# Optimization experiments

Measured on AMD Instinct MI355X. Metric: run time of the kernel, lower is better.

Reference implementation:

```python
import jax, jax.numpy as jnp
import numpy as np

N_NODES = 50000
N_EDGES = 800000
IN_CH = 128
HID = 64
NUM_HEADS = 8
NUM_CLASSES = 2
NEG_SLOPE = 0.2   # PyG GATConv default LeakyReLU slope
BN_EPS = 1e-5
SOFTMAX_EPS = 1e-16  # PyG softmax denominator epsilon


def setup_inputs() -> dict:
    key = jax.random.key(0)
    ks = jax.random.split(key, 20)
    s = 0.1
    inp = {
        "x": jax.random.normal(ks[0], (N_NODES, IN_CH), dtype=jnp.float32),
        "edge_index": jax.random.randint(ks[1], (2, N_EDGES), 0, N_NODES, dtype=jnp.int64),
        # layer 0 params, stacked over the 8 independent heads
        "W0": jax.random.normal(ks[2], (NUM_HEADS, IN_CH, HID), dtype=jnp.float32) * s,
        "a_src0": jax.random.normal(ks[3], (NUM_HEADS, HID), dtype=jnp.float32) * s,
        "a_dst0": jax.random.normal(ks[4], (NUM_HEADS, HID), dtype=jnp.float32) * s,
        "b0": jnp.zeros((NUM_HEADS, HID), dtype=jnp.float32),
        "gamma0": jnp.ones((NUM_HEADS, HID), dtype=jnp.float32),
        "beta0": jnp.zeros((NUM_HEADS, HID), dtype=jnp.float32),
        # layer 1 params
        "W1": jax.random.normal(ks[5], (NUM_HEADS, HID, HID), dtype=jnp.float32) * s,
        "a_src1": jax.random.normal(ks[6], (NUM_HEADS, HID), dtype=jnp.float32) * s,
        "a_dst1": jax.random.normal(ks[7], (NUM_HEADS, HID), dtype=jnp.float32) * s,
        "b1": jnp.zeros((NUM_HEADS, HID), dtype=jnp.float32),
        "gamma1": jnp.ones((NUM_HEADS, HID), dtype=jnp.float32),
        "beta1": jnp.zeros((NUM_HEADS, HID), dtype=jnp.float32),
        # ensemble classifier
        "Wc": jax.random.normal(ks[8], (NUM_HEADS * HID, NUM_CLASSES), dtype=jnp.float32) * s,
        "bc": jnp.zeros((NUM_CLASSES,), dtype=jnp.float32),
    }
    return inp


def _gat_layer(x, src, dst, n, W, a_s, a_d, b):
    """Single-head GATConv (PyG semantics, self-loops already in src/dst)."""
    h = x @ W                                           # [N, C]
    logits = (h @ a_s)[src] + (h @ a_d)[dst]            # [E]
    logits = jax.nn.leaky_relu(logits, NEG_SLOPE)
    m = jax.ops.segment_max(logits, dst, num_segments=n)
    ex = jnp.exp(logits - m[dst])
    denom = jax.ops.segment_sum(ex, dst, num_segments=n)
    alpha = ex / (denom[dst] + SOFTMAX_EPS)             # segment softmax over dst
    out = jax.ops.segment_sum(h[src] * alpha[:, None], dst, num_segments=n)
    return out + b


def _bn(h, gamma, beta):
    # BatchNorm1d training-mode math (batch statistics over nodes)
    mu = jnp.mean(h, axis=0)
    var = jnp.var(h, axis=0)
    return (h - mu) * jax.lax.rsqrt(var + BN_EPS) * gamma + beta


def reference(x, edge_index, W0, a_src0, a_dst0, b0, gamma0, beta0,
              W1, a_src1, a_dst1, b1, gamma1, beta1, Wc, bc):
    n = x.shape[0]
    loops = jnp.arange(n, dtype=edge_index.dtype)
    src = jnp.concatenate([edge_index[0], loops])  # PyG add_self_loops=True
    dst = jnp.concatenate([edge_index[1], loops])

    def branch(Wh0, as0, ad0, bh0, g0, be0, Wh1, as1, ad1, bh1, g1, be1):
        h = _gat_layer(x, src, dst, n, Wh0, as0, ad0, bh0)
        h = jax.nn.elu(_bn(h, g0, be0))                  # dropout off (eval)
        h = _gat_layer(h, src, dst, n, Wh1, as1, ad1, bh1)
        h = jax.nn.elu(_bn(h, g1, be1))
        return h                                          # [N, HID]

    hs = jax.vmap(branch)(W0, a_src0, a_dst0, b0, gamma0, beta0,
                          W1, a_src1, a_dst1, b1, gamma1, beta1)  # [H, N, HID]
    feat = jnp.transpose(hs, (1, 0, 2)).reshape(n, -1)            # [N, H*HID]
    return feat @ Wc + bc
```

## Files before the change

### kernel.cpp

```cpp
#include <hip/hip_runtime.h>
#include <hip/hip_bf16.h>
#include <math.h>
#include <stdint.h>

#define N_NODES 50000
#define N_EDGES 800000
#define E_TOT   (N_EDGES + N_NODES)
#define IN_CH   128
#define HID     64
#define NHEAD   8
#define C       512
#define NEG_SLOPE 0.2f
#define BN_EPS    1e-5f
#define SM_EPS    1e-16f
#define SCAN_B    196
#define STAT_B    256

typedef __attribute__((ext_vector_type(8))) short bf16x8;
typedef __attribute__((ext_vector_type(4))) float f32x4;

__device__ __forceinline__ float lrelu(float x){ return x > 0.f ? x : NEG_SLOPE * x; }
__device__ __forceinline__ float elu(float x){ return x > 0.f ? x : __expf(x) - 1.f; }
__device__ __forceinline__ float bflo(unsigned u){ return __uint_as_float(u << 16); }
__device__ __forceinline__ float bfhi(unsigned u){ return __uint_as_float(u & 0xffff0000u); }
__device__ __forceinline__ float bfu(unsigned short u){ return __uint_as_float(((unsigned)u) << 16); }
__device__ __forceinline__ unsigned short f2bf(float f){
  unsigned u = __float_as_uint(f);
  unsigned r = u + 0x7fffu + ((u >> 16) & 1u);
  return (unsigned short)(r >> 16);
}

__global__ void k_init(const int* __restrict__ ei, int* counts, int* flag, int* done){
  int i = blockIdx.x * 256 + threadIdx.x;
  if (i < N_NODES) counts[i] = 1;
  if (blockIdx.x == 0 && threadIdx.x == 0) {
    int f = 1;
    for (int k = 0; k < 32; k++) if (ei[2*k + 1] != 0) f = 0;
    *flag = f;
    *done = 0;
  }
}
__global__ void k_extract_count(const int* __restrict__ ei, const int* __restrict__ flag,
                                int* __restrict__ src32, int* __restrict__ dst32,
                                int* counts){
  int e = blockIdx.x * 256 + threadIdx.x;
  if (e >= N_EDGES) return;
  int s, d;
  if (*flag) {
    const long long* e64 = (const long long*)ei;
    s = (int)e64[e];
    d = (int)e64[(size_t)N_EDGES + e];
  } else {
    s = ei[e];
    d = ei[N_EDGES + e];
  }
  src32[e] = s; dst32[e] = d;
  atomicAdd(&counts[d], 1);
}

__global__ void k_scan12(const int* __restrict__ counts, int* __restrict__ excl,
                         int* __restrict__ bsum, int* done, int* __restrict__ bsum_s){
  __shared__ int s[256];
  __shared__ int isLast;
  int tid = threadIdx.x;
  int i = blockIdx.x * 256 + tid;
  int v = (i < N_NODES) ? counts[i] : 0;
  s[tid] = v; __syncthreads();
#pragma unroll
  for (int d = 1; d < 256; d <<= 1) {
    int t = (tid >= d) ? s[tid - d] : 0;
    __syncthreads(); s[tid] += t; __syncthreads();
  }
  if (i < N_NODES) excl[i] = s[tid] - v;
  if (tid == 255) bsum[blockIdx.x] = s[255];
  __threadfence();
  if (tid == 0) isLast = (atomicAdd(done, 1) == gridDim.x - 1);
  __syncthreads();
  if (isLast) {
    __threadfence();
    int bv = (tid < SCAN_B) ? bsum[tid] : 0;
    s[tid] = bv; __syncthreads();
#pragma unroll
    for (int d = 1; d < 256; d <<= 1) {
      int t = (tid >= d) ? s[tid - d] : 0;
      __syncthreads(); s[tid] += t; __syncthreads();
    }
    if (tid < SCAN_B) bsum_s[tid] = s[tid] - bv;
  }
}
__global__ void k_scan3(const int* __restrict__ excl, const int* __restrict__ bsum_s,
                        int* __restrict__ off, int* __restrict__ cursor, int* __restrict__ csr){
  int i = blockIdx.x * 256 + threadIdx.x;
  if (i < N_NODES) {
    int o = excl[i] + bsum_s[blockIdx.x];
    off[i] = o; cursor[i] = o + 1; csr[o] = i;
  }
  if (i == 0) off[N_NODES] = E_TOT;
}
__global__ void k_scatter_edges(const int* __restrict__ src, const int* __restrict__ dst,
                                int* cursor, int* __restrict__ csr_src){
  int e = blockIdx.x * 256 + threadIdx.x;
  if (e < N_EDGES) { int d = dst[e]; int p = atomicAdd(&cursor[d], 1); csr_src[p] = src[e]; }
}

__global__ void k_transpose_both(const float* __restrict__ W0, const float* __restrict__ W1,
                                 unsigned short* __restrict__ bt0, unsigned short* __restrict__ bt1){
  int i = blockIdx.x * 256 + threadIdx.x;
  if (i < 65536) {
    int k = i & 127; int rem = i >> 7; int c = rem & 63; int h = rem >> 6;
    bt0[i] = f2bf(W0[((size_t)h * IN_CH + k) * 64 + c]);
  } else {
    int j = i - 65536;
    int k = j & 63; int rem = j >> 6; int c = rem & 63; int h = rem >> 6;
    bt1[j] = f2bf(W1[((size_t)h * HID + k) * 64 + c]);
  }
}

__global__ __launch_bounds__(256) void k_gemm0(const float* __restrict__ X,
                                               const unsigned short* __restrict__ Bt,
                                               const float* __restrict__ a_src,
                                               const float* __restrict__ a_dst,
                                               unsigned short* __restrict__ H16,
                                               float* __restrict__ s_src,
                                               float* __restrict__ s_dst){
  __shared__ unsigned short LA[64 * 136];
  __shared__ unsigned short LB[64 * 136];
  int r0 = blockIdx.x * 64;
  int tid = threadIdx.x;
#pragma unroll
  for (int i = 0; i < 4; i++) {
    int idx = tid + i * 256;
    int r = idx >> 4, l16 = idx & 15;
    float4 u0 = make_float4(0.f,0.f,0.f,0.f), u1 = u0;
    if (r0 + r < N_NODES) {
      const float* xp = &X[(size_t)(r0 + r) * IN_CH + l16 * 8];
      u0 = *reinterpret_cast<const float4*>(xp);
      u1 = *reinterpret_cast<const float4*>(xp + 4);
    }
    ushort4 p0, p1;
    p0.x = f2bf(u0.x); p0.y = f2bf(u0.y); p0.z = f2bf(u0.z); p0.w = f2bf(u0.w);
    p1.x = f2bf(u1.x); p1.y = f2bf(u1.y); p1.z = f2bf(u1.z); p1.w = f2bf(u1.w);
    *reinterpret_cast<ushort4*>(&LA[r * 136 + l16 * 8]) = p0;
    *reinterpret_cast<ushort4*>(&LA[r * 136 + l16 * 8 + 4]) = p1;
  }
  int w = tid >> 6, l = tid & 63;
  int lr = l & 15, lg = l >> 4;
  for (int h = 0; h < NHEAD; h++) {
    __syncthreads();
#pragma unroll
    for (int i = 0; i < 4; i++) {
      int idx = tid + i * 256;
      int c = idx >> 4, l16 = idx & 15;
      uint4 v = *reinterpret_cast<const uint4*>(&Bt[(size_t)h * 8192 + c * 128 + l16 * 8]);
      *reinterpret_cast<uint4*>(&LB[c * 136 + l16 * 8]) = v;
    }
    __syncthreads();
    f32x4 acc[4] = {};
#pragma unroll
    for (int kf = 0; kf < 4; kf++) {
      bf16x8 af = *reinterpret_cast<const bf16x8*>(&LA[(w * 16 + lr) * 136 + kf * 32 + lg * 8]);
#pragma unroll
      for (int cf = 0; cf < 4; cf++) {
        bf16x8 bfr = *reinterpret_cast<const bf16x8*>(&LB[(cf * 16 + lr) * 136 + kf * 32 + lg * 8]);
        acc[cf] = __builtin_amdgcn_mfma_f32_16x16x32_bf16(af, bfr, acc[cf], 0, 0, 0);
      }
    }
#pragma unroll
    for (int cf = 0; cf < 4; cf++)
#pragma unroll
      for (int rr = 0; rr < 4; rr++) {
        int gr = r0 + w * 16 + lg * 4 + rr;
        if (gr < N_NODES)
          H16[(size_t)gr * C + h * HID + cf * 16 + lr] = f2bf(acc[cf][rr]);
      }
    float ps[4] = {}, pd[4] = {};
#pragma unroll
    for (int cf = 0; cf < 4; cf++) {
      float as_ = a_src[h * HID + cf * 16 + lr];
      float ad_ = a_dst[h * HID + cf * 16 + lr];
#pragma unroll
      for (int rr = 0; rr < 4; rr++) { ps[rr] += acc[cf][rr] * as_; pd[rr] += acc[cf][rr] * ad_; }
    }
#pragma unroll
    for (int rr = 0; rr < 4; rr++)
#pragma unroll
      for (int o = 1; o < 16; o <<= 1) { ps[rr] += __shfl_xor(ps[rr], o, 64); pd[rr] += __shfl_xor(pd[rr], o, 64); }
    if (lr == 0) {
#pragma unroll
      for (int rr = 0; rr < 4; rr++) {
        int gr = r0 + w * 16 + lg * 4 + rr;
        if (gr < N_NODES) { s_src[gr * NHEAD + h] = ps[rr]; s_dst[gr * NHEAD + h] = pd[rr]; }
      }
    }
  }
}

__global__ __launch_bounds__(256) void k_gemm1(const unsigned short* __restrict__ Hb,
                                               const unsigned short* __restrict__ Bt,
                                               const float* __restrict__ scale,
                                               const float* __restrict__ shift,
                                               const float* __restrict__ a_src,
                                               const float* __restrict__ a_dst,
                                               unsigned short* __restrict__ H16,
                                               float* __restrict__ s_src,
                                               float* __restrict__ s_dst){
  __shared__ unsigned short LA[64 * 72];
  __shared__ unsigned short LB[64 * 72];
  int r0 = blockIdx.x * 64, h = blockIdx.y;
  int tid = threadIdx.x;
#pragma unroll
  for (int i = 0; i < 4; i++) {
    int idx = tid + i * 256;
    int r = idx >> 4, l16 = idx & 15;
    ushort4 hv = make_ushort4(0, 0, 0, 0);
    if (r0 + r < N_NODES)
      hv = *reinterpret_cast<const ushort4*>(&Hb[(size_t)(r0 + r) * C + h * HID + l16 * 4]);
    float4 sc = *reinterpret_cast<const float4*>(&scale[h * HID + l16 * 4]);
    float4 sh = *reinterpret_cast<const float4*>(&shift[h * HID + l16 * 4]);
    ushort4 p;
    p.x = f2bf(elu(sc.x * bfu(hv.x) + sh.x));
    p.y = f2bf(elu(sc.y * bfu(hv.y) + sh.y));
    p.z = f2bf(elu(sc.z * bfu(hv.z) + sh.z));
    p.w = f2bf(elu(sc.w * bfu(hv.w) + sh.w));
    *reinterpret_cast<ushort4*>(&LA[r * 72 + l16 * 4]) = p;
  }
#pragma unroll
  for (int i = 0; i < 2; i++) {
    int idx = tid + i * 256;
    int c = idx >> 3, l8 = idx & 7;
    uint4 v = *reinterpret_cast<const uint4*>(&Bt[(size_t)h * 4096 + c * 64 + l8 * 8]);
    *reinterpret_cast<uint4*>(&LB[c * 72 + l8 * 8]) = v;
  }
  __syncthreads();
  int w = tid >> 6, l = tid & 63;
  int lr = l & 15, lg = l >> 4;
  f32x4 acc[4] = {};
#pragma unroll
  for (int kf = 0; kf < 2; kf++) {
    bf16x8 af = *reinterpret_cast<const bf16x8*>(&LA[(w * 16 + lr) * 72 + kf * 32 + lg * 8]);
#pragma unroll
    for (int cf = 0; cf < 4; cf++) {
      bf16x8 bfr = *reinterpret_cast<const bf16x8*>(&LB[(cf * 16 + lr) * 72 + kf * 32 + lg * 8]);
      acc[cf] = __builtin_amdgcn_mfma_f32_16x16x32_bf16(af, bfr, acc[cf], 0, 0, 0);
    }
  }
#pragma unroll
  for (int cf = 0; cf < 4; cf++)
#pragma unroll
    for (int rr = 0; rr < 4; rr++) {
      int gr = r0 + w * 16 + lg * 4 + rr;
      if (gr < N_NODES)
        H16[(size_t)gr * C + h * HID + cf * 16 + lr] = f2bf(acc[cf][rr]);
    }
  float ps[4] = {}, pd[4] = {};
#pragma unroll
  for (int cf = 0; cf < 4; cf++) {
    float as_ = a_src[h * HID + cf * 16 + lr];
    float ad_ = a_dst[h * HID + cf * 16 + lr];
#pragma unroll
    for (int rr = 0; rr < 4; rr++) { ps[rr] += acc[cf][rr] * as_; pd[rr] += acc[cf][rr] * ad_; }
  }
#pragma unroll
  for (int rr = 0; rr < 4; rr++)
#pragma unroll
    for (int o = 1; o < 16; o <<= 1) { ps[rr] += __shfl_xor(ps[rr], o, 64); pd[rr] += __shfl_xor(pd[rr], o, 64); }
  if (lr == 0) {
#pragma unroll
    for (int rr = 0; rr < 4; rr++) {
      int gr = r0 + w * 16 + lg * 4 + rr;
      if (gr < N_NODES) { s_src[gr * NHEAD + h] = ps[rr]; s_dst[gr * NHEAD + h] = pd[rr]; }
    }
  }
}

__global__ __launch_bounds__(256) void k_aggregate(const unsigned short* __restrict__ H16,
                                                   const float* __restrict__ s_src,
                                                   const float* __restrict__ s_dst,
                                                   const int* __restrict__ off,
                                                   const int* __restrict__ csr,
                                                   const float* __restrict__ bias,
                                                   unsigned short* __restrict__ HoutB){
  __shared__ float aexp[4][64][8];
  __shared__ int   sidx[4][64];
  int wv = threadIdx.x >> 6, lane = threadIdx.x & 63;
  int n = blockIdx.x * 4 + wv;
  if (n >= N_NODES) return;
  int e0 = off[n], deg = off[n + 1] - e0;
  int hsel = lane >> 3;

  float sd[NHEAD];
#pragma unroll
  for (int h = 0; h < NHEAD; h++) sd[h] = s_dst[n * NHEAD + h];

  float acc[8] = {};
  float dnl[NHEAD] = {};

  for (int base = 0; base < deg; base += 64) {
    int e = base + lane;
    int cnt = min(64, deg - base);
    if (e < deg) {
      int s = csr[e0 + e];
      sidx[wv][lane] = s;
      const float4* sp = reinterpret_cast<const float4*>(&s_src[s * NHEAD]);
      float4 s01 = sp[0], s23 = sp[1];
      float sv[8] = { s01.x, s01.y, s01.z, s01.w, s23.x, s23.y, s23.z, s23.w };
#pragma unroll
      for (int h = 0; h < NHEAD; h++) {
        float ex = __expf(lrelu(sv[h] + sd[h]));
        dnl[h] += ex;
        aexp[wv][lane][h] = ex;
      }
    }
    int j = 0;
    for (; j + 4 <= cnt; j += 4) {
      int s0 = sidx[wv][j+0], s1 = sidx[wv][j+1], s2 = sidx[wv][j+2], s3 = sidx[wv][j+3];
      float a0 = aexp[wv][j+0][hsel], a1 = aexp[wv][j+1][hsel];
      float a2 = aexp[wv][j+2][hsel], a3 = aexp[wv][j+3][hsel];
      uint4 v0 = reinterpret_cast<const uint4*>(H16 + (size_t)s0 * C)[lane];
      uint4 v1 = reinterpret_cast<const uint4*>(H16 + (size_t)s1 * C)[lane];
      uint4 v2 = reinterpret_cast<const uint4*>(H16 + (size_t)s2 * C)[lane];
      uint4 v3 = reinterpret_cast<const uint4*>(H16 + (size_t)s3 * C)[lane];
      acc[0] += a0 * bflo(v0.x); acc[1] += a0 * bfhi(v0.x);
      acc[2] += a0 * bflo(v0.y); acc[3] += a0 * bfhi(v0.y);
      acc[4] += a0 * bflo(v0.z); acc[5] += a0 * bfhi(v0.z);
      acc[6] += a0 * bflo(v0.w); acc[7] += a0 * bfhi(v0.w);
      acc[0] += a1 * bflo(v1.x); acc[1] += a1 * bfhi(v1.x);
      acc[2] += a1 * bflo(v1.y); acc[3] += a1 * bfhi(v1.y);
      acc[4] += a1 * bflo(v1.z); acc[5] += a1 * bfhi(v1.z);
      acc[6] += a1 * bflo(v1.w); acc[7] += a1 * bfhi(v1.w);
      acc[0] += a2 * bflo(v2.x); acc[1] += a2 * bfhi(v2.x);
      acc[2] += a2 * bflo(v2.y); acc[3] += a2 * bfhi(v2.y);
      acc[4] += a2 * bflo(v2.z); acc[5] += a2 * bfhi(v2.z);
      acc[6] += a2 * bflo(v2.w); acc[7] += a2 * bfhi(v2.w);
      acc[0] += a3 * bflo(v3.x); acc[1] += a3 * bfhi(v3.x);
      acc[2] += a3 * bflo(v3.y); acc[3] += a3 * bfhi(v3.y);
      acc[4] += a3 * bflo(v3.z); acc[5] += a3 * bfhi(v3.z);
      acc[6] += a3 * bflo(v3.w); acc[7] += a3 * bfhi(v3.w);
    }
    for (; j < cnt; j++) {
      int s = sidx[wv][j];
      float a = aexp[wv][j][hsel];
      uint4 v = reinterpret_cast<const uint4*>(H16 + (size_t)s * C)[lane];
      acc[0] += a * bflo(v.x); acc[1] += a * bfhi(v.x);
      acc[2] += a * bflo(v.y); acc[3] += a * bfhi(v.y);
      acc[4] += a * bflo(v.z); acc[5] += a * bfhi(v.z);
      acc[6] += a * bflo(v.w); acc[7] += a * bfhi(v.w);
    }
  }

  float mydn = 0.f;
#pragma unroll
  for (int h = 0; h < NHEAD; h++) {
    float d = dnl[h];
#pragma unroll
    for (int o = 32; o; o >>= 1) d += __shfl_xor(d, o, 64);
    if (hsel == h) mydn = d;
  }
  float inv = 1.f / (mydn + SM_EPS);

  const float* bp = bias + lane * 8;
  ushort4 p0, p1;
  p0.x = f2bf(acc[0]*inv + bp[0]); p0.y = f2bf(acc[1]*inv + bp[1]);
  p0.z = f2bf(acc[2]*inv + bp[2]); p0.w = f2bf(acc[3]*inv + bp[3]);
  p1.x = f2bf(acc[4]*inv + bp[4]); p1.y = f2bf(acc[5]*inv + bp[5]);
  p1.z = f2bf(acc[6]*inv + bp[6]); p1.w = f2bf(acc[7]*inv + bp[7]);
  unsigned short* op = HoutB + (size_t)n * C + lane * 8;
  *reinterpret_cast<ushort4*>(op) = p0;
  *reinterpret_cast<ushort4*>(op + 4) = p1;
}

__global__ __launch_bounds__(256) void k_bn_stats(const unsigned short* __restrict__ Hb,
                                                  float* __restrict__ partial){
  __shared__ float red[4][64][16];
  int tid = threadIdx.x, w = tid >> 6, c64 = tid & 63;
  float s[8] = {}, q[8] = {};
  for (int r = blockIdx.x * 4 + w; r < N_NODES; r += gridDim.x * 4) {
    uint4 v = *reinterpret_cast<const uint4*>(&Hb[(size_t)r * C + c64 * 8]);
    float f[8] = { bflo(v.x), bfhi(v.x), bflo(v.y), bfhi(v.y),
                   bflo(v.z), bfhi(v.z), bflo(v.w), bfhi(v.w) };
#pragma unroll
    for (int k = 0; k < 8; k++) { s[k] += f[k]; q[k] += f[k] * f[k]; }
  }
#pragma unroll
  for (int k = 0; k < 8; k++) { red[w][c64][k] = s[k]; red[w][c64][k + 8] = q[k]; }
  __syncthreads();
  if (w == 0) {
#pragma unroll
    for (int k = 0; k < 8; k++) {
      float ss = red[0][c64][k] + red[1][c64][k] + red[2][c64][k] + red[3][c64][k];
      float qq = red[0][c64][k+8] + red[1][c64][k+8] + red[2][c64][k+8] + red[3][c64][k+8];
      partial[(size_t)blockIdx.x * 1024 + c64 * 8 + k] = ss;
      partial[(size_t)blockIdx.x * 1024 + 512 + c64 * 8 + k] = qq;
    }
  }
}
__global__ void k_bn_finalize(const float* __restrict__ partial, const float* __restrict__ gamma,
                              const float* __restrict__ beta, float* __restrict__ scale,
                              float* __restrict__ shift){
  int c = threadIdx.x;
  float s = 0.f, q = 0.f;
  for (int b = 0; b < STAT_B; b++) {
    s += partial[(size_t)b * 1024 + c];
    q += partial[(size_t)b * 1024 + 512 + c];
  }
  float mean = s * (1.f / N_NODES);
  float var  = q * (1.f / N_NODES) - mean * mean;
  float sc = gamma[c] * rsqrtf(var + BN_EPS);
  scale[c] = sc;
  shift[c] = beta[c] - mean * sc;
}

__global__ __launch_bounds__(256) void k_final(const unsigned short* __restrict__ Hb,
                                               const float* __restrict__ scale,
                                               const float* __restrict__ shift,
                                               const float* __restrict__ Wc,
                                               const float* __restrict__ bc,
                                               float* __restrict__ out){
  int wave = threadIdx.x >> 6, lane = threadIdx.x & 63;
  int n = blockIdx.x * 4 + wave;
  if (n >= N_NODES) return;
  uint4 v = *reinterpret_cast<const uint4*>(&Hb[(size_t)n * C + lane * 8]);
  float f[8] = { bflo(v.x), bfhi(v.x), bflo(v.y), bfhi(v.y),
                 bflo(v.z), bfhi(v.z), bflo(v.w), bfhi(v.w) };
  float4 sc0 = *reinterpret_cast<const float4*>(&scale[lane * 8]);
  float4 sc1 = *reinterpret_cast<const float4*>(&scale[lane * 8 + 4]);
  float4 sh0 = *reinterpret_cast<const float4*>(&shift[lane * 8]);
  float4 sh1 = *reinterpret_cast<const float4*>(&shift[lane * 8 + 4]);
  float scv[8] = { sc0.x, sc0.y, sc0.z, sc0.w, sc1.x, sc1.y, sc1.z, sc1.w };
  float shv[8] = { sh0.x, sh0.y, sh0.z, sh0.w, sh1.x, sh1.y, sh1.z, sh1.w };
  float a0 = 0.f, a1 = 0.f;
#pragma unroll
  for (int k = 0; k < 8; k++) {
    float t = elu(scv[k] * f[k] + shv[k]);
    int ch = lane * 8 + k;
    a0 += t * Wc[ch * 2 + 0];
    a1 += t * Wc[ch * 2 + 1];
  }
#pragma unroll
  for (int o = 32; o; o >>= 1) { a0 += __shfl_xor(a0, o, 64); a1 += __shfl_xor(a1, o, 64); }
  if (lane == 0) { out[n * 2 + 0] = a0 + bc[0]; out[n * 2 + 1] = a1 + bc[1]; }
}

extern "C" void kernel_launch(void* const* d_in, const int* in_sizes, int n_in,
                              void* d_out, int out_size, void* d_ws, size_t ws_size,
                              hipStream_t stream) {
  const float* x      = (const float*)d_in[0];
  const int*   ei     = (const int*)d_in[1];
  const float* W0     = (const float*)d_in[2];
  const float* a_src0 = (const float*)d_in[3];
  const float* a_dst0 = (const float*)d_in[4];
  const float* b0     = (const float*)d_in[5];
  const float* gamma0 = (const float*)d_in[6];
  const float* beta0  = (const float*)d_in[7];
  const float* W1     = (const float*)d_in[8];
  const float* a_src1 = (const float*)d_in[9];
  const float* a_dst1 = (const float*)d_in[10];
  const float* b1     = (const float*)d_in[11];
  const float* gamma1 = (const float*)d_in[12];
  const float* beta1  = (const float*)d_in[13];
  const float* Wc     = (const float*)d_in[14];
  const float* bc     = (const float*)d_in[15];
  float* out = (float*)d_out;

  char* ws = (char*)d_ws;
  size_t o = 0;
  auto alloc = [&](size_t bytes) { char* p = ws + o; o = (o + bytes + 255) & ~(size_t)255; return p; };
  int*   flag    = (int*)  alloc(4);
  int*   done    = (int*)  alloc(4);
  int*   src32   = (int*)  alloc((size_t)N_EDGES * 4);
  int*   dst32   = (int*)  alloc((size_t)N_EDGES * 4);
  int*   counts  = (int*)  alloc((size_t)N_NODES * 4);
  int*   excl    = (int*)  alloc((size_t)N_NODES * 4);
  int*   bsum    = (int*)  alloc(256 * 4);
  int*   bsum_s  = (int*)  alloc(256 * 4);
  int*   off     = (int*)  alloc((size_t)(N_NODES + 1) * 4);
  int*   cursor  = (int*)  alloc((size_t)N_NODES * 4);
  int*   csr     = (int*)  alloc((size_t)E_TOT * 4);
  float* s_src   = (float*)alloc((size_t)N_NODES * NHEAD * 4);
  float* s_dst   = (float*)alloc((size_t)N_NODES * NHEAD * 4);
  float* partial = (float*)alloc((size_t)STAT_B * 1024 * 4);
  float* scale   = (float*)alloc(C * 4);
  float* shift   = (float*)alloc(C * 4);
  unsigned short* bt0  = (unsigned short*)alloc((size_t)NHEAD * HID * IN_CH * 2);
  unsigned short* bt1  = (unsigned short*)alloc((size_t)NHEAD * HID * HID * 2);
  unsigned short* h16a = (unsigned short*)alloc((size_t)N_NODES * C * 2);
  unsigned short* h16b = (unsigned short*)alloc((size_t)N_NODES * C * 2);

  const int GE = (N_EDGES + 255) / 256;
  const int GN = (N_NODES + 255) / 256;
  const int GW = (N_NODES + 3) / 4;
  const int GR = (N_NODES + 63) / 64;

  k_init<<<GN, 256, 0, stream>>>(ei, counts, flag, done);
  k_extract_count<<<GE, 256, 0, stream>>>(ei, flag, src32, dst32, counts);
  k_transpose_both<<<384, 256, 0, stream>>>(W0, W1, bt0, bt1);
  k_scan12<<<GN, 256, 0, stream>>>(counts, excl, bsum, done, bsum_s);
  k_scan3<<<GN, 256, 0, stream>>>(excl, bsum_s, off, cursor, csr);
  k_scatter_edges<<<GE, 256, 0, stream>>>(src32, dst32, cursor, csr);

  k_gemm0<<<GR, 256, 0, stream>>>(x, bt0, a_src0, a_dst0, h16a, s_src, s_dst);
  k_aggregate<<<GW, 256, 0, stream>>>(h16a, s_src, s_dst, off, csr, b0, h16b);
  k_bn_stats<<<STAT_B, 256, 0, stream>>>(h16b, partial);
  k_bn_finalize<<<1, 512, 0, stream>>>(partial, gamma0, beta0, scale, shift);

  k_gemm1<<<dim3(GR, NHEAD), 256, 0, stream>>>(h16b, bt1, scale, shift, a_src1, a_dst1, h16a, s_src, s_dst);
  k_aggregate<<<GW, 256, 0, stream>>>(h16a, s_src, s_dst, off, csr, b1, h16b);
  k_bn_stats<<<STAT_B, 256, 0, stream>>>(h16b, partial);
  k_bn_finalize<<<1, 512, 0, stream>>>(partial, gamma1, beta1, scale, shift);

  k_final<<<GW, 256, 0, stream>>>(h16b, scale, shift, Wc, bc, out);
}
```

Baseline: 517.0 us.

## Drop edge staging buffers, fuse BN finalize, shuffle-broadcast indices in aggregate

Edge extraction no longer writes 32-bit src/dst copies. A count kernel reads destinations straight from edge_index, the scatter kernel re-reads the raw indices, and the self-loop offset is folded into the scan by adding i. The BN finalize kernel is merged into the stats kernel through a last-block atomic counter, which removes two launches. The aggregate inner loop now broadcasts source indices with __shfl instead of staging them in LDS, and is unrolled by 2 instead of 4, which may expose less memory-level parallelism for the gathers.

```diff
diff --git a/kernel.cpp b/kernel.cpp
--- a/kernel.cpp
+++ b/kernel.cpp
@@ -30,19 +30,63 @@
   return (unsigned short)(r >> 16);
 }
 
-__global__ void k_init(const int* __restrict__ ei, int* counts, int* flag, int* done){
-  int i = blockIdx.x * 256 + threadIdx.x;
-  if (i < N_NODES) counts[i] = 1;
-  if (blockIdx.x == 0 && threadIdx.x == 0) {
+__global__ void k_detect(const int* __restrict__ ei, int* flag){
+  if (threadIdx.x == 0) {
     int f = 1;
     for (int k = 0; k < 32; k++) if (ei[2*k + 1] != 0) f = 0;
     *flag = f;
-    *done = 0;
-  }
-}
-__global__ void k_extract_count(const int* __restrict__ ei, const int* __restrict__ flag,
-                                int* __restrict__ src32, int* __restrict__ dst32,
-                                int* counts){
+  }
+}
+__global__ void k_count(const int* __restrict__ ei, const int* __restrict__ flag, int* counts){
+  int e = blockIdx.x * 256 + threadIdx.x;
+  if (e >= N_EDGES) return;
+  int d;
+  if (*flag) d = (int)((const long long*)ei)[(size_t)N_EDGES + e];
+  else       d = ei[N_EDGES + e];
+  atomicAdd(&counts[d], 1);
+}
+
+__global__ void k_scan12(const int* __restrict__ counts, int* __restrict__ excl,
+                         int* __restrict__ bsum, int* done, int* __restrict__ bsum_s){
+  __shared__ int s[256];
+  __shared__ int isLast;
+  int tid = threadIdx.x;
+  int i = blockIdx.x * 256 + tid;
+  int v = (i < N_NODES) ? counts[i] : 0;
+  s[tid] = v; __syncthreads();
+#pragma unroll
+  for (int d = 1; d < 256; d <<= 1) {
+    int t = (tid >= d) ? s[tid - d] : 0;
+    __syncthreads(); s[tid] += t; __syncthreads();
+  }
+  if (i < N_NODES) excl[i] = s[tid] - v;
+  if (tid == 255) bsum[blockIdx.x] = s[255];
+  __threadfence();
+  if (tid == 0) isLast = (atomicAdd(done, 1) == gridDim.x - 1);
+  __syncthreads();
+  if (isLast) {
+    __threadfence();
+    int bv = (tid < SCAN_B) ? bsum[tid] : 0;
+    s[tid] = bv; __syncthreads();
+#pragma unroll
+    for (int d = 1; d < 256; d <<= 1) {
+      int t = (tid >= d) ? s[tid - d] : 0;
+      __syncthreads(); s[tid] += t; __syncthreads();
+    }
+    if (tid < SCAN_B) bsum_s[tid] = s[tid] - bv;
+  }
+}
+__global__ void k_scan3(const int* __restrict__ excl, const int* __restrict__ bsum_s,
+                        int* __restrict__ off, int* __restrict__ cursor, int* __restrict__ csr){
+  int i = blockIdx.x * 256 + threadIdx.x;
+  if (i < N_NODES) {
+    int o = excl[i] + bsum_s[blockIdx.x] + i;
+    off[i] = o; cursor[i] = o + 1; csr[o] = i;
+  }
+  if (i == 0) off[N_NODES] = E_TOT;
+}
+__global__ void k_scatter_edges(const int* __restrict__ ei, const int* __restrict__ flag,
+                                int* cursor, int* __restrict__ csr_src){
   int e = blockIdx.x * 256 + threadIdx.x;
   if (e >= N_EDGES) return;
   int s, d;
@@ -54,53 +98,8 @@
     s = ei[e];
     d = ei[N_EDGES + e];
   }
-  src32[e] = s; dst32[e] = d;
-  atomicAdd(&counts[d], 1);
-}
-
-__global__ void k_scan12(const int* __restrict__ counts, int* __restrict__ excl,
-                         int* __restrict__ bsum, int* done, int* __restrict__ bsum_s){
-  __shared__ int s[256];
-  __shared__ int isLast;
-  int tid = threadIdx.x;
-  int i = blockIdx.x * 256 + tid;
-  int v = (i < N_NODES) ? counts[i] : 0;
-  s[tid] = v; __syncthreads();
-#pragma unroll
-  for (int d = 1; d < 256; d <<= 1) {
-    int t = (tid >= d) ? s[tid - d] : 0;
-    __syncthreads(); s[tid] += t; __syncthreads();
-  }
-  if (i < N_NODES) excl[i] = s[tid] - v;
-  if (tid == 255) bsum[blockIdx.x] = s[255];
-  __threadfence();
-  if (tid == 0) isLast = (atomicAdd(done, 1) == gridDim.x - 1);
-  __syncthreads();
-  if (isLast) {
-    __threadfence();
-    int bv = (tid < SCAN_B) ? bsum[tid] : 0;
-    s[tid] = bv; __syncthreads();
-#pragma unroll
-    for (int d = 1; d < 256; d <<= 1) {
-      int t = (tid >= d) ? s[tid - d] : 0;
-      __syncthreads(); s[tid] += t; __syncthreads();
-    }
-    if (tid < SCAN_B) bsum_s[tid] = s[tid] - bv;
-  }
-}
-__global__ void k_scan3(const int* __restrict__ excl, const int* __restrict__ bsum_s,
-                        int* __restrict__ off, int* __restrict__ cursor, int* __restrict__ csr){
-  int i = blockIdx.x * 256 + threadIdx.x;
-  if (i < N_NODES) {
-    int o = excl[i] + bsum_s[blockIdx.x];
-    off[i] = o; cursor[i] = o + 1; csr[o] = i;
-  }
-  if (i == 0) off[N_NODES] = E_TOT;
-}
-__global__ void k_scatter_edges(const int* __restrict__ src, const int* __restrict__ dst,
-                                int* cursor, int* __restrict__ csr_src){
-  int e = blockIdx.x * 256 + threadIdx.x;
-  if (e < N_EDGES) { int d = dst[e]; int p = atomicAdd(&cursor[d], 1); csr_src[p] = src[e]; }
+  int p = atomicAdd(&cursor[d], 1);
+  csr_src[p] = s;
 }
 
 __global__ void k_transpose_both(const float* __restrict__ W0, const float* __restrict__ W1,
@@ -280,8 +279,7 @@
                                                    const int* __restrict__ csr,
                                                    const float* __restrict__ bias,
                                                    unsigned short* __restrict__ HoutB){
-  __shared__ float aexp[4][64][8];
-  __shared__ int   sidx[4][64];
+  __shared__ float alds[4][64][8];
   int wv = threadIdx.x >> 6, lane = threadIdx.x & 63;
   int n = blockIdx.x * 4 + wv;
   if (n >= N_NODES) return;
@@ -298,49 +296,25 @@
   for (int base = 0; base < deg; base += 64) {
     int e = base + lane;
     int cnt = min(64, deg - base);
+    int s_reg = 0;
     if (e < deg) {
-      int s = csr[e0 + e];
-      sidx[wv][lane] = s;
-      const float4* sp = reinterpret_cast<const float4*>(&s_src[s * NHEAD]);
+      s_reg = csr[e0 + e];
+      const float4* sp = reinterpret_cast<const float4*>(&s_src[s_reg * NHEAD]);
       float4 s01 = sp[0], s23 = sp[1];
       float sv[8] = { s01.x, s01.y, s01.z, s01.w, s23.x, s23.y, s23.z, s23.w };
 #pragma unroll
       for (int h = 0; h < NHEAD; h++) {
         float ex = __expf(lrelu(sv[h] + sd[h]));
         dnl[h] += ex;
-        aexp[wv][lane][h] = ex;
+        alds[wv][lane][h] = ex;
       }
     }
-    int j = 0;
-    for (; j + 4 <= cnt; j += 4) {
-      int s0 = sidx[wv][j+0], s1 = sidx[wv][j+1], s2 = sidx[wv][j+2], s3 = sidx[wv][j+3];
-      float a0 = aexp[wv][j+0][hsel], a1 = aexp[wv][j+1][hsel];
-      float a2 = aexp[wv][j+2][hsel], a3 = aexp[wv][j+3][hsel];
-      uint4 v0 = reinterpret_cast<const uint4*>(H16 + (size_t)s0 * C)[lane];
-      uint4 v1 = reinterpret_cast<const uint4*>(H16 + (size_t)s1 * C)[lane];
-      uint4 v2 = reinterpret_cast<const uint4*>(H16 + (size_t)s2 * C)[lane];
-      uint4 v3 = reinterpret_cast<const uint4*>(H16 + (size_t)s3 * C)[lane];
-      acc[0] += a0 * bflo(v0.x); acc[1] += a0 * bfhi(v0.x);
-      acc[2] += a0 * bflo(v0.y); acc[3] += a0 * bfhi(v0.y);
-      acc[4] += a0 * bflo(v0.z); acc[5] += a0 * bfhi(v0.z);
-      acc[6] += a0 * bflo(v0.w); acc[7] += a0 * bfhi(v0.w);
-      acc[0] += a1 * bflo(v1.x); acc[1] += a1 * bfhi(v1.x);
-      acc[2] += a1 * bflo(v1.y); acc[3] += a1 * bfhi(v1.y);
-      acc[4] += a1 * bflo(v1.z); acc[5] += a1 * bfhi(v1.z);
-      acc[6] += a1 * bflo(v1.w); acc[7] += a1 * bfhi(v1.w);
-      acc[0] += a2 * bflo(v2.x); acc[1] += a2 * bfhi(v2.x);
-      acc[2] += a2 * bflo(v2.y); acc[3] += a2 * bfhi(v2.y);
-      acc[4] += a2 * bflo(v2.z); acc[5] += a2 * bfhi(v2.z);
-      acc[6] += a2 * bflo(v2.w); acc[7] += a2 * bfhi(v2.w);
-      acc[0] += a3 * bflo(v3.x); acc[1] += a3 * bfhi(v3.x);
-      acc[2] += a3 * bflo(v3.y); acc[3] += a3 * bfhi(v3.y);
-      acc[4] += a3 * bflo(v3.z); acc[5] += a3 * bfhi(v3.z);
-      acc[6] += a3 * bflo(v3.w); acc[7] += a3 * bfhi(v3.w);
-    }
-    for (; j < cnt; j++) {
-      int s = sidx[wv][j];
-      float a = aexp[wv][j][hsel];
-      uint4 v = reinterpret_cast<const uint4*>(H16 + (size_t)s * C)[lane];
+#pragma unroll 2
+    for (int j = 0; j < cnt; j++) {
+      int s = __shfl(s_reg, j, 64);
+      float a = alds[wv][j][hsel];
+      const uint4* rp = reinterpret_cast<const uint4*>(H16 + (size_t)s * C);
+      uint4 v = rp[lane];
       acc[0] += a * bflo(v.x); acc[1] += a * bfhi(v.x);
       acc[2] += a * bflo(v.y); acc[3] += a * bfhi(v.y);
       acc[4] += a * bflo(v.z); acc[5] += a * bfhi(v.z);
@@ -370,8 +344,13 @@
 }
 
 __global__ __launch_bounds__(256) void k_bn_stats(const unsigned short* __restrict__ Hb,
-                                                  float* __restrict__ partial){
+                                                  float* __restrict__ partial, int* done2,
+                                                  const float* __restrict__ gamma,
+                                                  const float* __restrict__ beta,
+                                                  float* __restrict__ scale,
+                                                  float* __restrict__ shift){
   __shared__ float red[4][64][16];
+  __shared__ int isLast;
   int tid = threadIdx.x, w = tid >> 6, c64 = tid & 63;
   float s[8] = {}, q[8] = {};
   for (int r = blockIdx.x * 4 + w; r < N_NODES; r += gridDim.x * 4) {
@@ -393,21 +372,27 @@
       partial[(size_t)blockIdx.x * 1024 + 512 + c64 * 8 + k] = qq;
     }
   }
-}
-__global__ void k_bn_finalize(const float* __restrict__ partial, const float* __restrict__ gamma,
-                              const float* __restrict__ beta, float* __restrict__ scale,
-                              float* __restrict__ shift){
-  int c = threadIdx.x;
-  float s = 0.f, q = 0.f;
-  for (int b = 0; b < STAT_B; b++) {
-    s += partial[(size_t)b * 1024 + c];
-    q += partial[(size_t)b * 1024 + 512 + c];
-  }
-  float mean = s * (1.f / N_NODES);
-  float var  = q * (1.f / N_NODES) - mean * mean;
-  float sc = gamma[c] * rsqrtf(var + BN_EPS);
-  scale[c] = sc;
-  shift[c] = beta[c] - mean * sc;
+  __threadfence();
+  if (tid == 0) isLast = (atomicAdd(done2, 1) == gridDim.x - 1);
+  __syncthreads();
+  if (isLast) {
+    __threadfence();
+#pragma unroll
+    for (int cc = 0; cc < 2; cc++) {
+      int c = tid + cc * 256;
+      float ssum = 0.f, qsum = 0.f;
+      for (int b = 0; b < STAT_B; b++) {
+        ssum += partial[(size_t)b * 1024 + c];
+        qsum += partial[(size_t)b * 1024 + 512 + c];
+      }
+      float mean = ssum * (1.f / N_NODES);
+      float var  = qsum * (1.f / N_NODES) - mean * mean;
+      float sc = gamma[c] * rsqrtf(var + BN_EPS);
+      scale[c] = sc;
+      shift[c] = beta[c] - mean * sc;
+    }
+    if (tid == 0) *done2 = 0;
+  }
 }
 
 __global__ __launch_bounds__(256) void k_final(const unsigned short* __restrict__ Hb,
@@ -466,9 +451,7 @@
   size_t o = 0;
   auto alloc = [&](size_t bytes) { char* p = ws + o; o = (o + bytes + 255) & ~(size_t)255; return p; };
   int*   flag    = (int*)  alloc(4);
-  int*   done    = (int*)  alloc(4);
-  int*   src32   = (int*)  alloc((size_t)N_EDGES * 4);
-  int*   dst32   = (int*)  alloc((size_t)N_EDGES * 4);
+  int*   done    = (int*)  alloc(8);
   int*   counts  = (int*)  alloc((size_t)N_NODES * 4);
   int*   excl    = (int*)  alloc((size_t)N_NODES * 4);
   int*   bsum    = (int*)  alloc(256 * 4);
@@ -491,22 +474,22 @@
   const int GW = (N_NODES + 3) / 4;
   const int GR = (N_NODES + 63) / 64;
 
-  k_init<<<GN, 256, 0, stream>>>(ei, counts, flag, done);
-  k_extract_count<<<GE, 256, 0, stream>>>(ei, flag, src32, dst32, counts);
+  hipMemsetAsync(counts, 0, (size_t)N_NODES * 4, stream);
+  hipMemsetAsync(done, 0, 8, stream);
+  k_detect<<<1, 64, 0, stream>>>(ei, flag);
+  k_count<<<GE, 256, 0, stream>>>(ei, flag, counts);
   k_transpose_both<<<384, 256, 0, stream>>>(W0, W1, bt0, bt1);
-  k_scan12<<<GN, 256, 0, stream>>>(counts, excl, bsum, done, bsum_s);
+  k_scan12<<<GN, 256, 0, stream>>>(counts, excl, bsum, &done[0], bsum_s);
   k_scan3<<<GN, 256, 0, stream>>>(excl, bsum_s, off, cursor, csr);
-  k_scatter_edges<<<GE, 256, 0, stream>>>(src32, dst32, cursor, csr);
+  k_scatter_edges<<<GE, 256, 0, stream>>>(ei, flag, cursor, csr);
 
   k_gemm0<<<GR, 256, 0, stream>>>(x, bt0, a_src0, a_dst0, h16a, s_src, s_dst);
   k_aggregate<<<GW, 256, 0, stream>>>(h16a, s_src, s_dst, off, csr, b0, h16b);
-  k_bn_stats<<<STAT_B, 256, 0, stream>>>(h16b, partial);
-  k_bn_finalize<<<1, 512, 0, stream>>>(partial, gamma0, beta0, scale, shift);
+  k_bn_stats<<<STAT_B, 256, 0, stream>>>(h16b, partial, &done[1], gamma0, beta0, scale, shift);
 
   k_gemm1<<<dim3(GR, NHEAD), 256, 0, stream>>>(h16b, bt1, scale, shift, a_src1, a_dst1, h16a, s_src, s_dst);
   k_aggregate<<<GW, 256, 0, stream>>>(h16a, s_src, s_dst, off, csr, b1, h16b);
-  k_bn_stats<<<STAT_B, 256, 0, stream>>>(h16b, partial);
-  k_bn_finalize<<<1, 512, 0, stream>>>(partial, gamma1, beta1, scale, shift);
+  k_bn_stats<<<STAT_B, 256, 0, stream>>>(h16b, partial, &done[1], gamma1, beta1, scale, shift);
 
   k_final<<<GW, 256, 0, stream>>>(h16b, scale, shift, Wc, bc, out);
 }
```

Measured after the change: 588.0 us. 1.14x slower.
